# Optimization experiments

Measured on AMD Instinct MI355X. Metric: run time of the kernel, lower is better.

## Reference

```python
import jax, jax.numpy as jnp
import numpy as np

POOL = 14  # pool_size


def setup_inputs() -> dict:
    key = jax.random.key(0)
    k1, k2, k3, k4, k5 = jax.random.split(key, 5)
    H = W = 128
    C = 1024
    R = 256  # num_rois
    img = jax.random.normal(k1, (1, H, W, C), dtype=jnp.float32)
    # valid integer boxes (x1,y1,x2,y2) with x2>x1, y2>y1, inside the map
    x1 = jax.random.randint(k2, (R,), 0, W // 2)
    y1 = jax.random.randint(k3, (R,), 0, H // 2)
    bw = jax.random.randint(k4, (R,), 4, W // 2)
    bh = jax.random.randint(k5, (R,), 4, H // 2)
    rois = jnp.stack([x1, y1, x1 + bw, y1 + bh], axis=1).astype(jnp.float32)[None]  # [1,R,4]
    return {"img": img, "rois": rois}


def _roi_resize(img, rois, pool):
    # img: [1,H,W,C], rois: [1,R,4] float (x1,y1,x2,y2)
    H, W = img.shape[1], img.shape[2]
    fmap = img[0]  # [H,W,C]
    r = rois[0].astype(jnp.int32)  # cast exactly as the Keras layer does
    x1, y1, x2, y2 = r[:, 0], r[:, 1], r[:, 2], r[:, 3]
    h = (y2 - y1).astype(jnp.float32)  # [R]
    w = (x2 - x1).astype(jnp.float32)
    i = jnp.arange(pool, dtype=jnp.float32)
    # TF1 resize_images bilinear, align_corners=False: src = dst * (in/out)
    src_y = i[None, :] * (h[:, None] / pool)  # [R,P]
    src_x = i[None, :] * (w[:, None] / pool)
    y0 = jnp.floor(src_y).astype(jnp.int32)
    x0 = jnp.floor(src_x).astype(jnp.int32)
    fy = src_y - y0.astype(jnp.float32)  # [R,P]
    fx = src_x - x0.astype(jnp.float32)
    y1i = jnp.minimum(y0 + 1, (y2 - y1)[:, None] - 1)  # clamp within crop
    x1i = jnp.minimum(x0 + 1, (x2 - x1)[:, None] - 1)
    # absolute indices into the feature map, clipped for safety
    ay0 = jnp.clip(y1[:, None] + y0, 0, H - 1)
    ay1 = jnp.clip(y1[:, None] + y1i, 0, H - 1)
    ax0 = jnp.clip(x1[:, None] + x0, 0, W - 1)
    ax1 = jnp.clip(x1[:, None] + x1i, 0, W - 1)
    # batched gather of the four bilinear corners: [R,P,P,C]
    v00 = fmap[ay0[:, :, None], ax0[:, None, :]]
    v01 = fmap[ay0[:, :, None], ax1[:, None, :]]
    v10 = fmap[ay1[:, :, None], ax0[:, None, :]]
    v11 = fmap[ay1[:, :, None], ax1[:, None, :]]
    fx_b = fx[:, None, :, None]  # [R,1,P,1]
    fy_b = fy[:, :, None, None]  # [R,P,1,1]
    top = v00 + (v01 - v00) * fx_b
    bot = v10 + (v11 - v10) * fx_b
    out = top + (bot - top) * fy_b  # [R,P,P,C]
    return out[None]  # [1,R,P,P,C]


def reference(img, rois):
    return _roi_resize(img, rois, POOL)
```

## Files before the change

kernel.cpp:

```cpp
#include <hip/hip_runtime.h>

#define POOL 14
#define IMG_H 128
#define IMG_W 128
#define IMG_C 1024
#define NROI 256

typedef __attribute__((ext_vector_type(4))) float float4v;

__global__ __launch_bounds__(256) void roi_resize_kernel(
    const float* __restrict__ img,
    const float* __restrict__ rois,
    float* __restrict__ out)
{
    const int d    = blockIdx.x;
    const int xcd  = d & 7;
    const int slot = d >> 3;
    const int rwi  = slot / POOL;
    const int i    = slot - rwi * POOL;
    const int r    = rwi * 8 + xcd;

    const int x1 = (int)rois[r * 4 + 0];
    const int y1 = (int)rois[r * 4 + 1];
    const int x2 = (int)rois[r * 4 + 2];
    const int y2 = (int)rois[r * 4 + 3];
    const int h = y2 - y1;
    const int w = x2 - x1;

    const float src_y = (float)i * ((float)h / (float)POOL);
    const int y0 = (int)floorf(src_y);
    const float fy = src_y - (float)y0;
    const int y1i = min(y0 + 1, h - 1);
    const int ay0 = min(max(y1 + y0,  0), IMG_H - 1);
    const int ay1 = min(max(y1 + y1i, 0), IMG_H - 1);

    const float* row0 = img + (size_t)(ay0 * IMG_W) * IMG_C;
    const float* row1 = img + (size_t)(ay1 * IMG_W) * IMG_C;

    const int c = threadIdx.x * 4;
    float* po = out + ((size_t)r * (POOL * POOL) + (size_t)i * POOL) * IMG_C + c;

    const float winv = (float)w / (float)POOL;

    #pragma unroll 2
    for (int j = 0; j < POOL; ++j) {
        const float src_x = (float)j * winv;
        const int x0 = (int)floorf(src_x);
        const float fx = src_x - (float)x0;
        const int x1i = min(x0 + 1, w - 1);
        const int ax0 = min(max(x1 + x0,  0), IMG_W - 1);
        const int ax1 = min(max(x1 + x1i, 0), IMG_W - 1);

        const float4v v00 = *(const float4v*)(row0 + (size_t)ax0 * IMG_C + c);
        const float4v v01 = *(const float4v*)(row0 + (size_t)ax1 * IMG_C + c);
        const float4v v10 = *(const float4v*)(row1 + (size_t)ax0 * IMG_C + c);
        const float4v v11 = *(const float4v*)(row1 + (size_t)ax1 * IMG_C + c);

        float4v o;
        #pragma unroll
        for (int k = 0; k < 4; ++k) {
            const float top = v00[k] + (v01[k] - v00[k]) * fx;
            const float bot = v10[k] + (v11[k] - v10[k]) * fx;
            o[k] = top + (bot - top) * fy;
        }
        __builtin_nontemporal_store(o, (float4v*)(po + (size_t)j * IMG_C));
    }
}

extern "C" void kernel_launch(void* const* d_in, const int* in_sizes, int n_in,
                              void* d_out, int out_size, void* d_ws, size_t ws_size,
                              hipStream_t stream) {
    const float* img  = (const float*)d_in[0];
    const float* rois = (const float*)d_in[1];
    float* out = (float*)d_out;

    const int blocks = NROI * POOL;
    roi_resize_kernel<<<blocks, 256, 0, stream>>>(img, rois, out);
}
```

Measured before the change: 298.5 us.

## Split work per ROI into channel slices mapped to XCDs with waves over pool cells

Each block now handles one ROI and one eighth of the channels, and its four waves loop over all 196 output cells. Before, each block handled one output row across all channels. The channel slice is chosen by block index mod 8, so each XCD's L2 caches only its own channel slice of the image. This is meant to raise L2 hit rates on the repeated corner gathers. The cost is narrower 8-byte loads and stores in place of 16-byte ones, fewer blocks (2048 instead of 3584), and a longer serial loop per wave.

New measurement: 305.2 us. 1.02x slower.

```diff
diff --git a/kernel.cpp b/kernel.cpp
--- a/kernel.cpp
+++ b/kernel.cpp
@@ -5,20 +5,21 @@
 #define IMG_W 128
 #define IMG_C 1024
 #define NROI 256
+#define NSLICE 8
+#define SLICE_C (IMG_C / NSLICE)
 
-typedef __attribute__((ext_vector_type(4))) float float4v;
+typedef __attribute__((ext_vector_type(2))) float float2v;
 
 __global__ __launch_bounds__(256) void roi_resize_kernel(
     const float* __restrict__ img,
     const float* __restrict__ rois,
     float* __restrict__ out)
 {
-    const int d    = blockIdx.x;
-    const int xcd  = d & 7;
-    const int slot = d >> 3;
-    const int rwi  = slot / POOL;
-    const int i    = slot - rwi * POOL;
-    const int r    = rwi * 8 + xcd;
+    const int d = blockIdx.x;
+    const int s = d & 7;
+    const int r = d >> 3;
+    const int lane = threadIdx.x & 63;
+    const int wv   = threadIdx.x >> 6;
 
     const int x1 = (int)rois[r * 4 + 0];
     const int y1 = (int)rois[r * 4 + 1];
@@ -26,44 +27,44 @@
     const int y2 = (int)rois[r * 4 + 3];
     const int h = y2 - y1;
     const int w = x2 - x1;
+    const float hdiv = (float)h / (float)POOL;
+    const float wdiv = (float)w / (float)POOL;
 
-    const float src_y = (float)i * ((float)h / (float)POOL);
-    const int y0 = (int)floorf(src_y);
-    const float fy = src_y - (float)y0;
-    const int y1i = min(y0 + 1, h - 1);
-    const int ay0 = min(max(y1 + y0,  0), IMG_H - 1);
-    const int ay1 = min(max(y1 + y1i, 0), IMG_H - 1);
+    const int cofs = s * SLICE_C + lane * 2;
+    const float* imgc = img + cofs;
+    float* outc = out + (size_t)r * (POOL * POOL) * IMG_C + cofs;
 
-    const float* row0 = img + (size_t)(ay0 * IMG_W) * IMG_C;
-    const float* row1 = img + (size_t)(ay1 * IMG_W) * IMG_C;
+    for (int it = 0; it < 49; ++it) {
+        const int p = it * 4 + wv;
+        const int i = p / POOL;
+        const int j = p - i * POOL;
 
-    const int c = threadIdx.x * 4;
-    float* po = out + ((size_t)r * (POOL * POOL) + (size_t)i * POOL) * IMG_C + c;
-
-    const float winv = (float)w / (float)POOL;
-
-    #pragma unroll 2
-    for (int j = 0; j < POOL; ++j) {
-        const float src_x = (float)j * winv;
+        const float src_y = (float)i * hdiv;
+        const float src_x = (float)j * wdiv;
+        const int y0 = (int)floorf(src_y);
         const int x0 = (int)floorf(src_x);
+        const float fy = src_y - (float)y0;
         const float fx = src_x - (float)x0;
+        const int y1i = min(y0 + 1, h - 1);
         const int x1i = min(x0 + 1, w - 1);
+        const int ay0 = min(max(y1 + y0,  0), IMG_H - 1);
+        const int ay1 = min(max(y1 + y1i, 0), IMG_H - 1);
         const int ax0 = min(max(x1 + x0,  0), IMG_W - 1);
         const int ax1 = min(max(x1 + x1i, 0), IMG_W - 1);
 
-        const float4v v00 = *(const float4v*)(row0 + (size_t)ax0 * IMG_C + c);
-        const float4v v01 = *(const float4v*)(row0 + (size_t)ax1 * IMG_C + c);
-        const float4v v10 = *(const float4v*)(row1 + (size_t)ax0 * IMG_C + c);
-        const float4v v11 = *(const float4v*)(row1 + (size_t)ax1 * IMG_C + c);
+        const float2v v00 = *(const float2v*)(imgc + (size_t)(ay0 * IMG_W + ax0) * IMG_C);
+        const float2v v01 = *(const float2v*)(imgc + (size_t)(ay0 * IMG_W + ax1) * IMG_C);
+        const float2v v10 = *(const float2v*)(imgc + (size_t)(ay1 * IMG_W + ax0) * IMG_C);
+        const float2v v11 = *(const float2v*)(imgc + (size_t)(ay1 * IMG_W + ax1) * IMG_C);
 
-        float4v o;
+        float2v o;
         #pragma unroll
-        for (int k = 0; k < 4; ++k) {
+        for (int k = 0; k < 2; ++k) {
             const float top = v00[k] + (v01[k] - v00[k]) * fx;
             const float bot = v10[k] + (v11[k] - v10[k]) * fx;
             o[k] = top + (bot - top) * fy;
         }
-        __builtin_nontemporal_store(o, (float4v*)(po + (size_t)j * IMG_C));
+        __builtin_nontemporal_store(o, (float2v*)(outc + (size_t)p * IMG_C));
     }
 }
 
@@ -74,6 +75,6 @@
     const float* rois = (const float*)d_in[1];
     float* out = (float*)d_out;
 
-    const int blocks = NROI * POOL;
+    const int blocks = NROI * NSLICE;
     roi_resize_kernel<<<blocks, 256, 0, stream>>>(img, rois, out);
 }
```
